# Kernel optimization log

Hardware: AMD Instinct MI355X
Metric: run time of the kernel (lower is better)

Reference implementation:

```python
import jax, jax.numpy as jnp
import numpy as np

DIM = 2048
N_HEAD = 32
N_KV = 8
HEAD_DIM = DIM // N_HEAD  # 64
GROUP = N_HEAD // N_KV    # 4


def setup_inputs() -> dict:
    key = jax.random.key(0)
    k1, k2, k3, k4 = jax.random.split(key, 4)
    B, S = 2, 2048
    x = jax.random.normal(k1, (B, S, DIM), dtype=jnp.float32)
    freqs_cis = jax.random.normal(k2, (S, HEAD_DIM // 2, 2), dtype=jnp.float32)
    wqkv_w = jax.random.normal(k3, (DIM, (N_HEAD + 2 * N_KV) * HEAD_DIM), dtype=jnp.float32) * 0.02
    wo_w = jax.random.normal(k4, (DIM, DIM), dtype=jnp.float32) * 0.02
    return {"x": x, "freqs_cis": freqs_cis, "wqkv_w": wqkv_w, "wo_w": wo_w}


def apply_rotary_emb(x, freqs_cis):
    # x: (B, S, H, head_dim), freqs_cis: (S, head_dim//2, 2)
    B, S, H, D = x.shape
    xs = x.astype(jnp.float32).reshape(B, S, H, D // 2, 2)
    fc = freqs_cis.reshape(1, S, 1, D // 2, 2)
    real = xs[..., 0] * fc[..., 0] - xs[..., 1] * fc[..., 1]
    imag = xs[..., 1] * fc[..., 0] + xs[..., 0] * fc[..., 1]
    out = jnp.stack([real, imag], axis=-1).reshape(B, S, H, D)
    return out.astype(x.dtype)


def reference(x, freqs_cis, wqkv_w, wo_w):
    B, S, _ = x.shape
    kv_size = N_KV * HEAD_DIM
    qkv = x @ wqkv_w  # (B, S, (n_head+2*n_kv)*head_dim)
    xq = qkv[..., :DIM].reshape(B, S, N_HEAD, HEAD_DIM)
    xk = qkv[..., DIM:DIM + kv_size].reshape(B, S, N_KV, HEAD_DIM)
    xv = qkv[..., DIM + kv_size:].reshape(B, S, N_KV, HEAD_DIM)

    xq = apply_rotary_emb(xq, freqs_cis)
    xk = apply_rotary_emb(xk, freqs_cis)

    # GQA without materializing repeated KV heads:
    # q: (B, n_kv, group, S, d); k, v: (B, n_kv, S, d)
    q = xq.transpose(0, 2, 1, 3).reshape(B, N_KV, GROUP, S, HEAD_DIM)
    k = xk.transpose(0, 2, 1, 3)
    v = xv.transpose(0, 2, 1, 3)

    scale = 1.0 / jnp.sqrt(jnp.asarray(HEAD_DIM, dtype=q.dtype))
    scores = jnp.einsum('bkgqd,bkKd->bkgqK', q, k) * scale  # (B, n_kv, group, S, S)
    causal = jnp.tril(jnp.ones((S, S), dtype=bool))
    neg = jnp.asarray(jnp.finfo(scores.dtype).min, dtype=scores.dtype)
    scores = jnp.where(causal, scores, neg)
    probs = jax.nn.softmax(scores, axis=-1)
    out = jnp.einsum('bkgqK,bkKd->bkgqd', probs, v)  # (B, n_kv, group, S, d)
    out = out.reshape(B, N_HEAD, S, HEAD_DIM).transpose(0, 2, 1, 3).reshape(B, S, DIM)
    return out @ wo_w
```

## Files before the change

### kernel.cpp

```cpp
#include <hip/hip_runtime.h>
#include <hip/hip_bf16.h>
#include <math.h>

#define DIM 2048
#define NH 32
#define NKV 8
#define HD 64
#define SEQ 2048
#define BATCH 2
#define MTOT (BATCH*SEQ)
#define QKV_N ((NH + 2*NKV)*HD)
#define QSCALE 0.18033688011112042f

typedef __bf16 bf16x8 __attribute__((ext_vector_type(8)));
typedef float f32x4 __attribute__((ext_vector_type(4)));

#if __has_builtin(__builtin_amdgcn_exp2f)
#define EXP2F __builtin_amdgcn_exp2f
#else
#define EXP2F exp2f
#endif

__device__ __forceinline__ void gld_lds16(const void* g, void* l) {
  __builtin_amdgcn_global_load_lds((__attribute__((address_space(1))) void*)g,
                                   (__attribute__((address_space(3))) void*)l,
                                   16, 0, 0);
}

#define PHASE_SYNC4 asm volatile("s_waitcnt vmcnt(4)\n\ts_barrier" ::: "memory")
#define PHASE_SYNC0 asm volatile("s_waitcnt vmcnt(0)\n\ts_barrier" ::: "memory")
#define POST_SYNC   asm volatile("s_waitcnt lgkmcnt(0)\n\ts_barrier" ::: "memory")

__global__ __launch_bounds__(256) void prologue_kernel(const float* __restrict__ x,
                                                       const float* __restrict__ wqkv,
                                                       const float* __restrict__ wo,
                                                       __hip_bfloat16* __restrict__ xb,
                                                       __hip_bfloat16* __restrict__ wqkvT,
                                                       __hip_bfloat16* __restrict__ woT) {
  __shared__ float tile[32][33];
  const int id = blockIdx.x;
  if (id < 8192) {
    const int i = id * 256 + threadIdx.x;
    float4 v = ((const float4*)x)[i];
    union { __hip_bfloat16 h[4]; uint2 u; } t;
    t.h[0] = __float2bfloat16(v.x); t.h[1] = __float2bfloat16(v.y);
    t.h[2] = __float2bfloat16(v.z); t.h[3] = __float2bfloat16(v.w);
    ((uint2*)xb)[i] = t.u;
    return;
  }
  const float* src;
  __hip_bfloat16* dst;
  int C, bx, by;
  if (id < 8192 + 6144) {
    const int r = id - 8192;
    src = wqkv; dst = wqkvT; C = QKV_N;
    bx = r % 96; by = r / 96;
  } else {
    const int r = id - (8192 + 6144);
    src = wo; dst = woT; C = DIM;
    bx = r & 63; by = r >> 6;
  }
  const int R = DIM;
  const int c0 = bx * 32, r0 = by * 32;
  const int tx = threadIdx.x & 31, ty = threadIdx.x >> 5;
  #pragma unroll
  for (int i = ty; i < 32; i += 8)
    tile[i][tx] = src[(size_t)(r0 + i) * C + c0 + tx];
  __syncthreads();
  #pragma unroll
  for (int i = ty; i < 32; i += 8)
    dst[(size_t)(c0 + i) * R + r0 + tx] = __float2bfloat16(tile[tx][i]);
}

__global__ __launch_bounds__(256) void gemm_qkv_rope_kernel(const __hip_bfloat16* __restrict__ A,
                                                            const __hip_bfloat16* __restrict__ Bt,
                                                            const float* __restrict__ freqs,
                                                            __hip_bfloat16* __restrict__ Qb,
                                                            __hip_bfloat16* __restrict__ Kb,
                                                            __hip_bfloat16* __restrict__ Vb) {
  __shared__ __hip_bfloat16 As[2][128 * 32];
  __shared__ __hip_bfloat16 Bs[2][128 * 32];
  const int tid = threadIdx.x;
  const int w = tid >> 6, lane = tid & 63, ln = lane & 15, quad = lane >> 4;
  const int wr = w >> 1, wc = w & 1;
  const int id = blockIdx.x;
  const int wg = (id & 7) * 96 + (id >> 3);
  const int bx = wg % 24, by = wg / 24;
  const int m0 = by * 128, n0 = bx * 128;
  const int K = DIM;
  const __hip_bfloat16* Ag = A + (size_t)(m0 + w * 16 + (lane >> 2)) * K + (lane & 3) * 8;
  const __hip_bfloat16* Bg = Bt + (size_t)(n0 + w * 16 + (lane >> 2)) * K + (lane & 3) * 8;
  f32x4 acc[4][4] = {};

  auto stage = [&](int buf, int k) {
    gld_lds16(Ag + k, &As[buf][w * 512]);
    gld_lds16(Ag + (size_t)64 * K + k, &As[buf][w * 512 + 2048]);
    gld_lds16(Bg + k, &Bs[buf][w * 512]);
    gld_lds16(Bg + (size_t)64 * K + k, &Bs[buf][w * 512 + 2048]);
  };
  auto compute = [&](int buf) {
    bf16x8 af[4], bf[4];
    #pragma unroll
    for (int i = 0; i < 4; i++)
      af[i] = *(const bf16x8*)&As[buf][(wr * 64 + i * 16 + ln) * 32 + quad * 8];
    #pragma unroll
    for (int j = 0; j < 4; j++)
      bf[j] = *(const bf16x8*)&Bs[buf][(wc * 64 + j * 16 + ln) * 32 + quad * 8];
    #pragma unroll
    for (int i = 0; i < 4; i++)
      #pragma unroll
      for (int j = 0; j < 4; j++)
        acc[i][j] = __builtin_amdgcn_mfma_f32_16x16x32_bf16(af[i], bf[j], acc[i][j], 0, 0, 0);
  };

  stage(0, 0);
  stage(1, 32);
  for (int k0 = 0; k0 + 64 < K; k0 += 64) {
    PHASE_SYNC4;
    compute(0);
    POST_SYNC;
    stage(0, k0 + 64);
    PHASE_SYNC4;
    compute(1);
    POST_SYNC;
    stage(1, k0 + 96);
  }
  PHASE_SYNC4;
  compute(0);
  PHASE_SYNC0;
  compute(1);

  const int region = (n0 >= 2560) ? 2 : (n0 >= 2048 ? 1 : 0);
  #pragma unroll
  for (int i = 0; i < 4; i++) {
    #pragma unroll
    for (int j = 0; j < 4; j++) {
      const int n = n0 + wc * 64 + j * 16 + ln;
      const int d = n & 63;
      #pragma unroll
      for (int r = 0; r < 4; r++) {
        const int m = m0 + wr * 64 + i * 16 + quad * 4 + r;
        const int bb = m >> 11, s = m & 2047;
        float v = acc[i][j][r];
        if (region == 2) {
          Vb[((size_t)(bb * NKV + ((n - 2560) >> 6)) * SEQ + s) * HD + d] = __float2bfloat16(v);
        } else {
          float p = __shfl_xor(v, 1);
          const float2 fc = *(const float2*)&freqs[s * 64 + (d & ~1)];
          float o = (d & 1) ? (v * fc.x + p * fc.y) : (v * fc.x - p * fc.y);
          if (region == 0)
            Qb[((size_t)(bb * NH + (n >> 6)) * SEQ + s) * HD + d] = __float2bfloat16(o * QSCALE);
          else
            Kb[((size_t)(bb * NKV + ((n - 2048) >> 6)) * SEQ + s) * HD + d] = __float2bfloat16(o);
        }
      }
    }
  }
}

__global__ __launch_bounds__(256) void gemm_wo_kernel(const __hip_bfloat16* __restrict__ A,
                                                      const __hip_bfloat16* __restrict__ Bt,
                                                      float* __restrict__ C) {
  __shared__ __hip_bfloat16 As[2][128 * 32];
  __shared__ __hip_bfloat16 Bs[2][128 * 32];
  const int tid = threadIdx.x;
  const int w = tid >> 6, lane = tid & 63, ln = lane & 15, quad = lane >> 4;
  const int wr = w >> 1, wc = w & 1;
  const int id = blockIdx.x;
  const int wg = (id & 7) * 64 + (id >> 3);
  const int bx = wg & 15, by = wg >> 4;
  const int m0 = by * 128, n0 = bx * 128;
  const int K = DIM, N = DIM;
  const __hip_bfloat16* Ag = A + (size_t)(m0 + w * 16 + (lane >> 2)) * K + (lane & 3) * 8;
  const __hip_bfloat16* Bg = Bt + (size_t)(n0 + w * 16 + (lane >> 2)) * K + (lane & 3) * 8;
  f32x4 acc[4][4] = {};

  auto stage = [&](int buf, int k) {
    gld_lds16(Ag + k, &As[buf][w * 512]);
    gld_lds16(Ag + (size_t)64 * K + k, &As[buf][w * 512 + 2048]);
    gld_lds16(Bg + k, &Bs[buf][w * 512]);
    gld_lds16(Bg + (size_t)64 * K + k, &Bs[buf][w * 512 + 2048]);
  };
  auto compute = [&](int buf) {
    bf16x8 af[4], bf[4];
    #pragma unroll
    for (int i = 0; i < 4; i++)
      af[i] = *(const bf16x8*)&As[buf][(wr * 64 + i * 16 + ln) * 32 + quad * 8];
    #pragma unroll
    for (int j = 0; j < 4; j++)
      bf[j] = *(const bf16x8*)&Bs[buf][(wc * 64 + j * 16 + ln) * 32 + quad * 8];
    #pragma unroll
    for (int i = 0; i < 4; i++)
      #pragma unroll
      for (int j = 0; j < 4; j++)
        acc[i][j] = __builtin_amdgcn_mfma_f32_16x16x32_bf16(af[i], bf[j], acc[i][j], 0, 0, 0);
  };

  stage(0, 0);
  stage(1, 32);
  for (int k0 = 0; k0 + 64 < K; k0 += 64) {
    PHASE_SYNC4;
    compute(0);
    POST_SYNC;
    stage(0, k0 + 64);
    PHASE_SYNC4;
    compute(1);
    POST_SYNC;
    stage(1, k0 + 96);
  }
  PHASE_SYNC4;
  compute(0);
  PHASE_SYNC0;
  compute(1);

  #pragma unroll
  for (int i = 0; i < 4; i++) {
    const int r0 = m0 + wr * 64 + i * 16 + quad * 4;
    #pragma unroll
    for (int j = 0; j < 4; j++) {
      const int cc = n0 + wc * 64 + j * 16 + ln;
      #pragma unroll
      for (int r = 0; r < 4; r++)
        C[(size_t)(r0 + r) * N + cc] = acc[i][j][r];
    }
  }
}

__global__ __launch_bounds__(256, 3) void attn_kernel(const __hip_bfloat16* __restrict__ Q,
                                                      const __hip_bfloat16* __restrict__ Kg,
                                                      const __hip_bfloat16* __restrict__ Vg,
                                                      __hip_bfloat16* __restrict__ O) {
  __shared__ __hip_bfloat16 Ks[128 * 64];
  __shared__ __hip_bfloat16 Vs[64 * 136];
  __shared__ __hip_bfloat16 Ps[4][32 * 72];
  const int id = blockIdx.x;
  const int xcd = id & 7, slot = id >> 3;
  const int cmb = xcd * 2 + (slot >> 6);
  const int b = cmb >> 3, kvh = cmb & 7;
  const int s_ = slot & 63;
  const int t = 15 - (s_ >> 2);
  const int h = kvh * 4 + (s_ & 3);
  const int tid = threadIdx.x, w = tid >> 6, lane = tid & 63, ln = lane & 15, quad = lane >> 4;
  const size_t qbase = (size_t)(b * NH + h) * SEQ * HD;
  const size_t kbase = (size_t)(b * NKV + kvh) * SEQ * HD;

  const __hip_bfloat16* Kgl = Kg + kbase + (size_t)(tid >> 3) * 64 + (size_t)(((tid & 7) ^ ((tid >> 3) & 7)) * 8);
  const int vrow = tid >> 2, vcb = (tid & 3) * 16, vsw = (tid & 3) << 4;
  const int psw = ((ln >> 2) & 3) << 4;

  const int qgw = t * 128 + w * 32;
  bf16x8 qf[2][2];
  #pragma unroll
  for (int f = 0; f < 2; f++)
    #pragma unroll
    for (int kt = 0; kt < 2; kt++)
      qf[f][kt] = *(const bf16x8*)(Q + qbase + (size_t)(qgw + f * 16 + ln) * HD + kt * 32 + quad * 8);
  f32x4 Oacc[2][4] = {};
  float lrow[2][4] = {};
  union { unsigned short u[8]; bf16x8 v; } onesu;
  #pragma unroll
  for (int i = 0; i < 8; i++) onesu.u[i] = 0x3F80;
  const bf16x8 ones = onesu.v;

  uint4 vd[2][2];
  #pragma unroll
  for (int bt = 0; bt < 2; bt++)
    #pragma unroll
    for (int cc = 0; cc < 2; cc++)
      vd[bt][cc] = *(const uint4*)(Vg + kbase + (size_t)(bt * 64 + vrow) * HD + vcb + cc * 8);

  for (int j = 0; j <= t; j++) {
    #pragma unroll
    for (int c = 0; c < 4; c++)
      gld_lds16(Kgl + (size_t)j * 8192 + c * 2048, &Ks[c * 2048 + w * 512]);
    #pragma unroll
    for (int bt = 0; bt < 2; bt++)
      #pragma unroll
      for (int cc = 0; cc < 2; cc++) {
        const __hip_bfloat16* vp = (const __hip_bfloat16*)&vd[bt][cc];
        const int col = vcb + cc * 8;
        const int sr = (bt * 64 + vrow) ^ vsw;
        #pragma unroll
        for (int e = 0; e < 8; e++)
          Vs[(col + e) * 136 + sr] = vp[e];
      }
    __syncthreads();
    if (j < t) {
      #pragma unroll
      for (int bt = 0; bt < 2; bt++)
        #pragma unroll
        for (int cc = 0; cc < 2; cc++)
          vd[bt][cc] = *(const uint4*)(Vg + kbase + (size_t)((j + 1) * 128 + bt * 64 + vrow) * HD + vcb + cc * 8);
    }
    const bool lastIter = (j == t);
    #pragma unroll
    for (int s2 = 0; s2 < 2; s2++) {
      if (lastIter && s2 * 64 > w * 32 + 31) continue;
      bf16x8 kf[4][2];
      #pragma unroll
      for (int nt = 0; nt < 4; nt++)
        #pragma unroll
        for (int kt = 0; kt < 2; kt++) {
          const int kv = s2 * 64 + nt * 16 + ln;
          kf[nt][kt] = *(const bf16x8*)&Ks[(kv * 8 + ((kt * 4 + quad) ^ (ln & 7))) * 8];
        }
      #pragma unroll
      for (int f = 0; f < 2; f++) {
        if (lastIter && s2 * 64 > w * 32 + f * 16 + 15) continue;
        f32x4 sf[4];
        #pragma unroll
        for (int nt = 0; nt < 4; nt++) {
          f32x4 s = {};
          s = __builtin_amdgcn_mfma_f32_16x16x32_bf16(kf[nt][0], qf[f][0], s, 0, 0, 0);
          s = __builtin_amdgcn_mfma_f32_16x16x32_bf16(kf[nt][1], qf[f][1], s, 0, 0, 0);
          sf[nt] = s;
        }
        if (lastIter && s2 * 64 + 63 > w * 32 + f * 16) {
          const int qv = w * 32 + f * 16 + ln;
          #pragma unroll
          for (int nt = 0; nt < 4; nt++) {
            const int kg = s2 * 64 + nt * 16 + quad * 4;
            #pragma unroll
            for (int r = 0; r < 4; r++)
              if (kg + r > qv) sf[nt][r] = -1.0e38f;
          }
        }
        #pragma unroll
        for (int nt = 0; nt < 4; nt++) {
          union { __hip_bfloat16 h[4]; uint2 u; } pk;
          #pragma unroll
          for (int r = 0; r < 4; r++)
            pk.h[r] = __float2bfloat16(EXP2F(sf[nt][r]));
          *(uint2*)&Ps[w][(f * 16 + ln) * 72 + ((nt * 16 + quad * 4) ^ psw)] = pk.u;
        }
      }
      f32x4 lsa[2] = {};
      #pragma unroll
      for (int kt = 0; kt < 2; kt++) {
        bf16x8 vfr[4];
        #pragma unroll
        for (int dt = 0; dt < 4; dt++)
          vfr[dt] = *(const bf16x8*)&Vs[(dt * 16 + ln) * 136 + s2 * 64 + ((kt * 32 + quad * 8) ^ (dt << 4))];
        #pragma unroll
        for (int f = 0; f < 2; f++) {
          if (lastIter && s2 * 64 > w * 32 + f * 16 + 15) continue;
          bf16x8 pf = *(const bf16x8*)&Ps[w][(f * 16 + ln) * 72 + ((kt * 32 + quad * 8) ^ psw)];
          lsa[f] = __builtin_amdgcn_mfma_f32_16x16x32_bf16(pf, ones, lsa[f], 0, 0, 0);
          #pragma unroll
          for (int dt = 0; dt < 4; dt++)
            Oacc[f][dt] = __builtin_amdgcn_mfma_f32_16x16x32_bf16(pf, vfr[dt], Oacc[f][dt], 0, 0, 0);
        }
      }
      #pragma unroll
      for (int f = 0; f < 2; f++) {
        if (lastIter && s2 * 64 > w * 32 + f * 16 + 15) continue;
        #pragma unroll
        for (int r = 0; r < 4; r++) lrow[f][r] += lsa[f][r];
      }
    }
    __syncthreads();
  }
  #pragma unroll
  for (int f = 0; f < 2; f++) {
    const int so = qgw + f * 16 + quad * 4;
    #pragma unroll
    for (int r = 0; r < 4; r++) {
      const float inv = 1.0f / lrow[f][r];
      #pragma unroll
      for (int dt = 0; dt < 4; dt++)
        O[((size_t)(b * SEQ) + so + r) * DIM + h * HD + dt * 16 + ln] =
            __float2bfloat16(Oacc[f][dt][r] * inv);
    }
  }
}

extern "C" void kernel_launch(void* const* d_in, const int* in_sizes, int n_in,
                              void* d_out, int out_size, void* d_ws, size_t ws_size,
                              hipStream_t stream) {
  const float* x     = (const float*)d_in[0];
  const float* freqs = (const float*)d_in[1];
  const float* wqkv  = (const float*)d_in[2];
  const float* wo    = (const float*)d_in[3];
  float* out = (float*)d_out;

  char* ws = (char*)d_ws;
  __hip_bfloat16* xb    = (__hip_bfloat16*)ws; ws += (size_t)MTOT * DIM * 2;
  __hip_bfloat16* wqkvT = (__hip_bfloat16*)ws; ws += (size_t)QKV_N * DIM * 2;
  __hip_bfloat16* woT   = (__hip_bfloat16*)ws; ws += (size_t)DIM * DIM * 2;
  __hip_bfloat16* Qb    = (__hip_bfloat16*)ws; ws += (size_t)BATCH * NH * SEQ * HD * 2;
  __hip_bfloat16* Kb    = (__hip_bfloat16*)ws; ws += (size_t)BATCH * NKV * SEQ * HD * 2;
  __hip_bfloat16* Vb    = (__hip_bfloat16*)ws; ws += (size_t)BATCH * NKV * SEQ * HD * 2;
  __hip_bfloat16* attnb = (__hip_bfloat16*)ws; ws += (size_t)MTOT * DIM * 2;

  prologue_kernel<<<8192 + 6144 + 4096, 256, 0, stream>>>(x, wqkv, wo, xb, wqkvT, woT);
  gemm_qkv_rope_kernel<<<768, 256, 0, stream>>>(xb, wqkvT, freqs, Qb, Kb, Vb);
  attn_kernel<<<1024, 256, 0, stream>>>(Qb, Kb, Vb, attnb);
  gemm_wo_kernel<<<512, 256, 0, stream>>>(attnb, woT, out);
}
```

Measured before the change: 299.4 us.

## Halve attention KV tile to 64 rows, raise occupancy, and rebalance causal block order

The attention kernel now stages 64-key K/V tiles in LDS instead of 128-key tiles. This roughly halves shared memory per block and lets launch bounds request 4 blocks per CU instead of 3. The causal skip is now computed per 64-key tile against each wave's query range, replacing the special last-iteration handling. The q-tile ordering changes from strictly longest-first to an interleaved pattern, presumably to balance work across co-resident blocks. The cost is twice as many loop iterations and barriers per block.

```diff
diff --git a/kernel.cpp b/kernel.cpp
--- a/kernel.cpp
+++ b/kernel.cpp
@@ -226,19 +226,20 @@
   }
 }
 
-__global__ __launch_bounds__(256, 3) void attn_kernel(const __hip_bfloat16* __restrict__ Q,
+__global__ __launch_bounds__(256, 4) void attn_kernel(const __hip_bfloat16* __restrict__ Q,
                                                       const __hip_bfloat16* __restrict__ Kg,
                                                       const __hip_bfloat16* __restrict__ Vg,
                                                       __hip_bfloat16* __restrict__ O) {
-  __shared__ __hip_bfloat16 Ks[128 * 64];
-  __shared__ __hip_bfloat16 Vs[64 * 136];
+  __shared__ __hip_bfloat16 Ks[64 * 64];
+  __shared__ __hip_bfloat16 Vs[64 * 72];
   __shared__ __hip_bfloat16 Ps[4][32 * 72];
   const int id = blockIdx.x;
   const int xcd = id & 7, slot = id >> 3;
   const int cmb = xcd * 2 + (slot >> 6);
   const int b = cmb >> 3, kvh = cmb & 7;
   const int s_ = slot & 63;
-  const int t = 15 - (s_ >> 2);
+  const int u = s_ >> 2;
+  const int t = (u < 8) ? u : 23 - u;
   const int h = kvh * 4 + (s_ & 3);
   const int tid = threadIdx.x, w = tid >> 6, lane = tid & 63, ln = lane & 15, quad = lane >> 4;
   const size_t qbase = (size_t)(b * NH + h) * SEQ * HD;
@@ -262,51 +263,44 @@
   for (int i = 0; i < 8; i++) onesu.u[i] = 0x3F80;
   const bf16x8 ones = onesu.v;
 
-  uint4 vd[2][2];
-  #pragma unroll
-  for (int bt = 0; bt < 2; bt++)
-    #pragma unroll
-    for (int cc = 0; cc < 2; cc++)
-      vd[bt][cc] = *(const uint4*)(Vg + kbase + (size_t)(bt * 64 + vrow) * HD + vcb + cc * 8);
-
-  for (int j = 0; j <= t; j++) {
-    #pragma unroll
-    for (int c = 0; c < 4; c++)
-      gld_lds16(Kgl + (size_t)j * 8192 + c * 2048, &Ks[c * 2048 + w * 512]);
-    #pragma unroll
-    for (int bt = 0; bt < 2; bt++)
-      #pragma unroll
-      for (int cc = 0; cc < 2; cc++) {
-        const __hip_bfloat16* vp = (const __hip_bfloat16*)&vd[bt][cc];
-        const int col = vcb + cc * 8;
-        const int sr = (bt * 64 + vrow) ^ vsw;
-        #pragma unroll
-        for (int e = 0; e < 8; e++)
-          Vs[(col + e) * 136 + sr] = vp[e];
-      }
+  const int jmax = 2 * t + 1;
+  uint4 vd[2];
+  #pragma unroll
+  for (int cc = 0; cc < 2; cc++)
+    vd[cc] = *(const uint4*)(Vg + kbase + (size_t)vrow * HD + vcb + cc * 8);
+
+  for (int j = 0; j <= jmax; j++) {
+    #pragma unroll
+    for (int c = 0; c < 2; c++)
+      gld_lds16(Kgl + (size_t)j * 4096 + c * 2048, &Ks[c * 2048 + w * 512]);
+    #pragma unroll
+    for (int cc = 0; cc < 2; cc++) {
+      const __hip_bfloat16* vp = (const __hip_bfloat16*)&vd[cc];
+      const int col = vcb + cc * 8;
+      const int sr = vrow ^ vsw;
+      #pragma unroll
+      for (int e = 0; e < 8; e++)
+        Vs[(col + e) * 72 + sr] = vp[e];
+    }
     __syncthreads();
-    if (j < t) {
-      #pragma unroll
-      for (int bt = 0; bt < 2; bt++)
-        #pragma unroll
-        for (int cc = 0; cc < 2; cc++)
-          vd[bt][cc] = *(const uint4*)(Vg + kbase + (size_t)((j + 1) * 128 + bt * 64 + vrow) * HD + vcb + cc * 8);
-    }
-    const bool lastIter = (j == t);
-    #pragma unroll
-    for (int s2 = 0; s2 < 2; s2++) {
-      if (lastIter && s2 * 64 > w * 32 + 31) continue;
+    if (j < jmax) {
+      #pragma unroll
+      for (int cc = 0; cc < 2; cc++)
+        vd[cc] = *(const uint4*)(Vg + kbase + (size_t)((j + 1) * 64 + vrow) * HD + vcb + cc * 8);
+    }
+    const int kb = j * 64;
+    if (kb <= qgw + 31) {
       bf16x8 kf[4][2];
       #pragma unroll
       for (int nt = 0; nt < 4; nt++)
         #pragma unroll
         for (int kt = 0; kt < 2; kt++) {
-          const int kv = s2 * 64 + nt * 16 + ln;
+          const int kv = nt * 16 + ln;
           kf[nt][kt] = *(const bf16x8*)&Ks[(kv * 8 + ((kt * 4 + quad) ^ (ln & 7))) * 8];
         }
       #pragma unroll
       for (int f = 0; f < 2; f++) {
-        if (lastIter && s2 * 64 > w * 32 + f * 16 + 15) continue;
+        if (kb > qgw + f * 16 + 15) continue;
         f32x4 sf[4];
         #pragma unroll
         for (int nt = 0; nt < 4; nt++) {
@@ -315,11 +309,11 @@
           s = __builtin_amdgcn_mfma_f32_16x16x32_bf16(kf[nt][1], qf[f][1], s, 0, 0, 0);
           sf[nt] = s;
         }
-        if (lastIter && s2 * 64 + 63 > w * 32 + f * 16) {
-          const int qv = w * 32 + f * 16 + ln;
+        if (kb + 63 > qgw + f * 16) {
+          const int qv = qgw + f * 16 + ln;
           #pragma unroll
           for (int nt = 0; nt < 4; nt++) {
-            const int kg = s2 * 64 + nt * 16 + quad * 4;
+            const int kg = kb + nt * 16 + quad * 4;
             #pragma unroll
             for (int r = 0; r < 4; r++)
               if (kg + r > qv) sf[nt][r] = -1.0e38f;
@@ -340,10 +334,10 @@
         bf16x8 vfr[4];
         #pragma unroll
         for (int dt = 0; dt < 4; dt++)
-          vfr[dt] = *(const bf16x8*)&Vs[(dt * 16 + ln) * 136 + s2 * 64 + ((kt * 32 + quad * 8) ^ (dt << 4))];
+          vfr[dt] = *(const bf16x8*)&Vs[(dt * 16 + ln) * 72 + ((kt * 32 + quad * 8) ^ (dt << 4))];
         #pragma unroll
         for (int f = 0; f < 2; f++) {
-          if (lastIter && s2 * 64 > w * 32 + f * 16 + 15) continue;
+          if (kb > qgw + f * 16 + 15) continue;
           bf16x8 pf = *(const bf16x8*)&Ps[w][(f * 16 + ln) * 72 + ((kt * 32 + quad * 8) ^ psw)];
           lsa[f] = __builtin_amdgcn_mfma_f32_16x16x32_bf16(pf, ones, lsa[f], 0, 0, 0);
           #pragma unroll
@@ -353,7 +347,7 @@
       }
       #pragma unroll
       for (int f = 0; f < 2; f++) {
-        if (lastIter && s2 * 64 > w * 32 + f * 16 + 15) continue;
+        if (kb > qgw + f * 16 + 15) continue;
         #pragma unroll
         for (int r = 0; r < 4; r++) lrow[f][r] += lsa[f][r];
       }
```

After: 363.7 us. 1.21x slower.
